# Kernel optimization log

Measured on AMD Instinct MI355X. Metric: run time of the kernel, lower is better.

Reference implementation:

```python
import jax, jax.numpy as jnp
import numpy as np

N_TOKEN = 256
C_PAIR = 128
C = 32
N_HEADS = 4
LN_EPS = 1e-5


def setup_inputs() -> dict:
    key = jax.random.key(0)
    ks = jax.random.split(key, 8)
    w = lambda k, shape: jax.random.normal(k, shape, dtype=jnp.float32) * 0.02
    return {
        "pair": jax.random.normal(ks[0], (N_TOKEN, N_TOKEN, C_PAIR), dtype=jnp.float32),
        "gamma": jnp.ones((C_PAIR,), dtype=jnp.float32),
        "beta": jnp.zeros((C_PAIR,), dtype=jnp.float32),
        "Wq": w(ks[1], (C_PAIR, C * N_HEADS)),
        "Wk": w(ks[2], (C_PAIR, C * N_HEADS)),
        "Wv": w(ks[3], (C_PAIR, C * N_HEADS)),
        "Wb": w(ks[4], (C_PAIR, N_HEADS)),
        "Wg": w(ks[5], (C_PAIR, C * N_HEADS)),
        "Wout": w(ks[6], (C * N_HEADS, C_PAIR)),
    }


def _layernorm(x, gamma, beta):
    mu = jnp.mean(x, axis=-1, keepdims=True)
    var = jnp.mean(jnp.square(x - mu), axis=-1, keepdims=True)
    return (x - mu) * jax.lax.rsqrt(var + LN_EPS) * gamma + beta


def reference(pair, gamma, beta, Wq, Wk, Wv, Wb, Wg, Wout):
    n = pair.shape[0]
    pn = _layernorm(pair, gamma, beta)  # [N, N, c_pair]
    q = (pn @ Wq).reshape(n, n, N_HEADS, C)  # [i, j, h, c]
    k = (pn @ Wk).reshape(n, n, N_HEADS, C)  # [i, k, h, c]
    v = (pn @ Wv).reshape(n, n, N_HEADS, C)
    b = pn @ Wb                               # [j, k, h] pairwise bias
    g = jax.nn.sigmoid(pn @ Wg).reshape(n, n, N_HEADS, C)
    # a^h_ijk = softmax_k( q_ij . k_ik / sqrt(c) + b_jk )
    logits = jnp.einsum("ijhc,ikhc->ijkh", q, k) / np.float32(np.sqrt(C))
    logits = logits + b[None, :, :, :]        # broadcast over i: bias indexed by (j, k)
    attn = jax.nn.softmax(logits, axis=2)     # softmax over k axis
    o = jnp.einsum("ijkh,ikhc->ijhc", attn, v) * g
    return o.reshape(n, n, N_HEADS * C) @ Wout  # [N, N, c_pair]
```

## Files before the change

### kernel.cpp

```cpp
#include <hip/hip_runtime.h>

#define N_TOK 256
#define CP    128
#define CHD   32
#define NH    4
#define NT    65536
#define NCOL  528

typedef short short8 __attribute__((ext_vector_type(8)));
typedef float f32x4  __attribute__((ext_vector_type(4)));

__device__ __forceinline__ short f2bf(float f) {
    unsigned u = __builtin_bit_cast(unsigned, f);
    u += 0x7fffu + ((u >> 16) & 1u);
    return (short)(u >> 16);
}
__device__ __forceinline__ float bf2f(short s) {
    unsigned u = ((unsigned)(unsigned short)s) << 16;
    return __builtin_bit_cast(float, u);
}

__global__ void pack_weights(const float* __restrict__ Wq, const float* __restrict__ Wk,
                             const float* __restrict__ Wv, const float* __restrict__ Wb,
                             const float* __restrict__ Wg, const float* __restrict__ Wout,
                             short* __restrict__ wcat, short* __restrict__ woutT) {
    int idx = blockIdx.x * 256 + threadIdx.x;
    if (idx < NCOL * CP) {
        int n = idx >> 7, k = idx & 127;
        float v = 0.f;
        if (n < 512) {
            const float* W = (n < 128) ? Wq : (n < 256) ? Wk : (n < 384) ? Wv : Wg;
            v = W[k * 128 + (n & 127)];
        } else if (n < 516) {
            v = Wb[k * 4 + (n - 512)];
        }
        wcat[n * CP + k] = f2bf(v);
    } else {
        int j = idx - NCOL * CP;
        if (j < 128 * 128) {
            int n = j >> 7, k = j & 127;
            woutT[n * 128 + k] = f2bf(Wout[k * 128 + n]);
        }
    }
}

__global__ __launch_bounds__(256)
void ln_proj(const float* __restrict__ pair, const float* __restrict__ gamma,
             const float* __restrict__ beta, const short* __restrict__ wcat,
             short* __restrict__ qt, short* __restrict__ kt,
             short* __restrict__ vt, short* __restrict__ gt,
             float* __restrict__ bt) {
    __shared__ short pn[64 * 136];
    const int tid = threadIdx.x;
    const int wv = tid >> 6, lane = tid & 63;
    const int quad = lane >> 4, l15 = lane & 15;
    const int r0 = blockIdx.x * 64;

    float ga0 = gamma[2 * lane], ga1 = gamma[2 * lane + 1];
    float be0 = beta[2 * lane],  be1 = beta[2 * lane + 1];

    #pragma unroll 4
    for (int rr = 0; rr < 16; ++rr) {
        int row = wv * 16 + rr;
        const float* src = pair + (size_t)(r0 + row) * CP + 2 * lane;
        float x0 = src[0], x1 = src[1];
        float s = x0 + x1;
        #pragma unroll
        for (int m = 32; m; m >>= 1) s += __shfl_xor(s, m);
        float mu = s * (1.f / 128.f);
        float d0 = x0 - mu, d1 = x1 - mu;
        float vs = d0 * d0 + d1 * d1;
        #pragma unroll
        for (int m = 32; m; m >>= 1) vs += __shfl_xor(vs, m);
        float rs = rsqrtf(vs * (1.f / 128.f) + 1e-5f);
        short y0 = f2bf(d0 * rs * ga0 + be0);
        short y1 = f2bf(d1 * rs * ga1 + be1);
        unsigned pk = ((unsigned)(unsigned short)y0) | (((unsigned)(unsigned short)y1) << 16);
        *(unsigned*)&pn[row * 136 + 2 * lane] = pk;
    }
    __syncthreads();

    short8 afrag[4];
    #pragma unroll
    for (int s = 0; s < 4; ++s)
        afrag[s] = *(const short8*)&pn[(wv * 16 + l15) * 136 + s * 32 + quad * 8];

    for (int ch = 0; ch < 33; ++ch) {
        int n = ch * 16 + l15;
        f32x4 acc = {0.f, 0.f, 0.f, 0.f};
        #pragma unroll
        for (int s = 0; s < 4; ++s) {
            short8 bfrag = *(const short8*)&wcat[(size_t)n * CP + s * 32 + quad * 8];
            acc = __builtin_amdgcn_mfma_f32_16x16x32_bf16(afrag[s], bfrag, acc, 0, 0, 0);
        }
        if (ch < 32) {
            int arr = n >> 7;
            int h = (n >> 5) & 3, c = n & 31;
            short* dst = (arr == 0) ? qt : (arr == 1) ? kt : (arr == 2) ? vt : gt;
            size_t base = (size_t)h * NT * CHD + c;
            #pragma unroll
            for (int r = 0; r < 4; ++r) {
                int gr = r0 + wv * 16 + quad * 4 + r;
                float val = acc[r];
                if (arr == 3) val = 1.f / (1.f + __expf(-val));
                dst[base + (size_t)gr * CHD] = f2bf(val);
            }
        } else if (l15 < 4) {
            int h = l15;
            #pragma unroll
            for (int r = 0; r < 4; ++r) {
                int gr = r0 + wv * 16 + quad * 4 + r;
                bt[h * NT + gr] = acc[r];
            }
        }
    }
}

__global__ __launch_bounds__(256)
void attn(const short* __restrict__ qt, const short* __restrict__ kt,
          const short* __restrict__ vt, const short* __restrict__ gt,
          const float* __restrict__ bt, short* __restrict__ og) {
    __shared__ short vT[32 * 264];
    __shared__ short pl[64 * 264];
    const int tid = threadIdx.x;
    const int h = blockIdx.x >> 8, i = blockIdx.x & 255;
    const int wv = tid >> 6, lane = tid & 63;
    const int quad = lane >> 4, l15 = lane & 15;

    const short* kbase = kt + ((size_t)h * NT + (size_t)i * 256) * CHD;
    const short* vbase = vt + ((size_t)h * NT + (size_t)i * 256) * CHD;
    const short* qbase = qt + ((size_t)h * NT + (size_t)i * 256) * CHD;
    const short* gbase = gt + ((size_t)h * NT + (size_t)i * 256) * CHD;
    const float* bbase = bt + (size_t)h * NT;

    for (int g = tid; g < 1024; g += 256) {
        int key = g >> 2, p = g & 3;
        short8 s = *(const short8*)(vbase + key * CHD + p * 8);
        #pragma unroll
        for (int cc = 0; cc < 8; ++cc)
            vT[(p * 8 + cc) * 264 + key] = s[cc];
    }
    __syncthreads();

    const float scale = 0.17677669529663687f;

    for (int jt = 0; jt < 4; ++jt) {
        int jbase = jt * 64 + wv * 16;
        short8 aq = *(const short8*)(qbase + (jbase + l15) * CHD + quad * 8);

        f32x4 sacc[16];
        #pragma unroll
        for (int t = 0; t < 16; ++t) {
            short8 bk = *(const short8*)(kbase + (t * 16 + l15) * CHD + quad * 8);
            f32x4 z = {0.f, 0.f, 0.f, 0.f};
            sacc[t] = __builtin_amdgcn_mfma_f32_16x16x32_bf16(aq, bk, z, 0, 0, 0);
        }
        #pragma unroll
        for (int t = 0; t < 16; ++t)
            #pragma unroll
            for (int r = 0; r < 4; ++r) {
                int j = jbase + quad * 4 + r;
                sacc[t][r] = sacc[t][r] * scale + bbase[(size_t)j * 256 + t * 16 + l15];
            }
        float mx[4] = {-1e30f, -1e30f, -1e30f, -1e30f}, sm[4] = {0.f, 0.f, 0.f, 0.f};
        #pragma unroll
        for (int t = 0; t < 16; ++t)
            #pragma unroll
            for (int r = 0; r < 4; ++r) mx[r] = fmaxf(mx[r], sacc[t][r]);
        #pragma unroll
        for (int m = 1; m < 16; m <<= 1)
            #pragma unroll
            for (int r = 0; r < 4; ++r) mx[r] = fmaxf(mx[r], __shfl_xor(mx[r], m, 16));
        #pragma unroll
        for (int t = 0; t < 16; ++t)
            #pragma unroll
            for (int r = 0; r < 4; ++r) {
                float e = __expf(sacc[t][r] - mx[r]);
                sacc[t][r] = e;
                sm[r] += e;
            }
        #pragma unroll
        for (int m = 1; m < 16; m <<= 1)
            #pragma unroll
            for (int r = 0; r < 4; ++r) sm[r] += __shfl_xor(sm[r], m, 16);
        float inv[4];
        #pragma unroll
        for (int r = 0; r < 4; ++r) inv[r] = 1.f / sm[r];
        #pragma unroll
        for (int t = 0; t < 16; ++t)
            #pragma unroll
            for (int r = 0; r < 4; ++r)
                pl[(wv * 16 + quad * 4 + r) * 264 + t * 16 + l15] = f2bf(sacc[t][r] * inv[r]);
        __syncthreads();
        f32x4 oacc[2];
        oacc[0] = f32x4{0.f, 0.f, 0.f, 0.f};
        oacc[1] = f32x4{0.f, 0.f, 0.f, 0.f};
        #pragma unroll
        for (int ks = 0; ks < 8; ++ks) {
            short8 ap = *(const short8*)&pl[(wv * 16 + l15) * 264 + ks * 32 + quad * 8];
            #pragma unroll
            for (int nt = 0; nt < 2; ++nt) {
                short8 bv = *(const short8*)&vT[(nt * 16 + l15) * 264 + ks * 32 + quad * 8];
                oacc[nt] = __builtin_amdgcn_mfma_f32_16x16x32_bf16(ap, bv, oacc[nt], 0, 0, 0);
            }
        }
        #pragma unroll
        for (int nt = 0; nt < 2; ++nt) {
            int c = nt * 16 + l15;
            #pragma unroll
            for (int r = 0; r < 4; ++r) {
                int j = jbase + quad * 4 + r;
                float gv = bf2f(gbase[(size_t)j * CHD + c]);
                float o = oacc[nt][r] * gv;
                og[((size_t)i * 256 + j) * CP + h * CHD + c] = f2bf(o);
            }
        }
        __syncthreads();
    }
}

__global__ __launch_bounds__(256)
void out_gemm(const short* __restrict__ og, const short* __restrict__ woutT,
              float* __restrict__ out) {
    __shared__ short al[64 * 136];
    const int tid = threadIdx.x;
    const int wv = tid >> 6, lane = tid & 63;
    const int quad = lane >> 4, l15 = lane & 15;
    const int r0 = blockIdx.x * 64;

    for (int g = tid; g < 1024; g += 256) {
        int row = g >> 4, p = g & 15;
        *(short8*)&al[row * 136 + p * 8] = *(const short8*)(og + (size_t)(r0 + row) * CP + p * 8);
    }
    __syncthreads();

    short8 af[4];
    #pragma unroll
    for (int s = 0; s < 4; ++s)
        af[s] = *(const short8*)&al[(wv * 16 + l15) * 136 + s * 32 + quad * 8];

    #pragma unroll
    for (int ch = 0; ch < 8; ++ch) {
        int n = ch * 16 + l15;
        f32x4 acc = {0.f, 0.f, 0.f, 0.f};
        #pragma unroll
        for (int s = 0; s < 4; ++s) {
            short8 bfrag = *(const short8*)&woutT[(size_t)n * 128 + s * 32 + quad * 8];
            acc = __builtin_amdgcn_mfma_f32_16x16x32_bf16(af[s], bfrag, acc, 0, 0, 0);
        }
        #pragma unroll
        for (int r = 0; r < 4; ++r)
            out[(size_t)(r0 + wv * 16 + quad * 4 + r) * CP + n] = acc[r];
    }
}

extern "C" void kernel_launch(void* const* d_in, const int* in_sizes, int n_in,
                              void* d_out, int out_size, void* d_ws, size_t ws_size,
                              hipStream_t stream) {
    (void)in_sizes; (void)n_in; (void)out_size; (void)ws_size;
    const float* pair  = (const float*)d_in[0];
    const float* gamma = (const float*)d_in[1];
    const float* beta  = (const float*)d_in[2];
    const float* Wq    = (const float*)d_in[3];
    const float* Wk    = (const float*)d_in[4];
    const float* Wv    = (const float*)d_in[5];
    const float* Wb    = (const float*)d_in[6];
    const float* Wg    = (const float*)d_in[7];
    const float* Wout  = (const float*)d_in[8];
    float* out = (float*)d_out;

    char* ws = (char*)d_ws;
    const size_t SZ_QKVG = (size_t)NH * NT * CHD * 2;
    short* wcat  = (short*)(ws);
    short* woutT = (short*)(ws + 135168);
    short* qt    = (short*)(ws + 167936);
    short* kt    = (short*)(ws + 167936 + SZ_QKVG);
    short* vt    = (short*)(ws + 167936 + 2 * SZ_QKVG);
    short* gt    = (short*)(ws + 167936 + 3 * SZ_QKVG);
    float* bt    = (float*)(ws + 167936 + 4 * SZ_QKVG);
    short* og    = (short*)(ws + 167936 + 4 * SZ_QKVG + (size_t)NH * NT * 4);

    hipLaunchKernelGGL(pack_weights, dim3(328), dim3(256), 0, stream,
                       Wq, Wk, Wv, Wb, Wg, Wout, wcat, woutT);
    hipLaunchKernelGGL(ln_proj, dim3(1024), dim3(256), 0, stream,
                       pair, gamma, beta, wcat, qt, kt, vt, gt, bt);
    hipLaunchKernelGGL(attn, dim3(1024), dim3(256), 0, stream,
                       qt, kt, vt, gt, bt, og);
    hipLaunchKernelGGL(out_gemm, dim3(1024), dim3(256), 0, stream,
                       og, woutT, out);
}
```

Baseline: 227.0 us.

## Split projection columns across waves and double-buffer weight fragments in ln_proj

Result: faster. 211.1 us (-7.0%).

```diff
diff --git a/kernel.cpp b/kernel.cpp
--- a/kernel.cpp
+++ b/kernel.cpp
@@ -44,7 +44,7 @@
     }
 }
 
-__global__ __launch_bounds__(256)
+__global__ __launch_bounds__(256, 4)
 void ln_proj(const float* __restrict__ pair, const float* __restrict__ gamma,
              const float* __restrict__ beta, const short* __restrict__ wcat,
              short* __restrict__ qt, short* __restrict__ kt,
@@ -80,40 +80,72 @@
     }
     __syncthreads();
 
-    short8 afrag[4];
+    short8 af[4][4];
     #pragma unroll
-    for (int s = 0; s < 4; ++s)
-        afrag[s] = *(const short8*)&pn[(wv * 16 + l15) * 136 + s * 32 + quad * 8];
-
-    for (int ch = 0; ch < 33; ++ch) {
-        int n = ch * 16 + l15;
-        f32x4 acc = {0.f, 0.f, 0.f, 0.f};
-        #pragma unroll
-        for (int s = 0; s < 4; ++s) {
-            short8 bfrag = *(const short8*)&wcat[(size_t)n * CP + s * 32 + quad * 8];
-            acc = __builtin_amdgcn_mfma_f32_16x16x32_bf16(afrag[s], bfrag, acc, 0, 0, 0);
-        }
-        if (ch < 32) {
-            int arr = n >> 7;
-            int h = (n >> 5) & 3, c = n & 31;
-            short* dst = (arr == 0) ? qt : (arr == 1) ? kt : (arr == 2) ? vt : gt;
-            size_t base = (size_t)h * NT * CHD + c;
-            #pragma unroll
-            for (int r = 0; r < 4; ++r) {
-                int gr = r0 + wv * 16 + quad * 4 + r;
-                float val = acc[r];
-                if (arr == 3) val = 1.f / (1.f + __expf(-val));
-                dst[base + (size_t)gr * CHD] = f2bf(val);
-            }
-        } else if (l15 < 4) {
-            int h = l15;
-            #pragma unroll
-            for (int r = 0; r < 4; ++r) {
-                int gr = r0 + wv * 16 + quad * 4 + r;
-                bt[h * NT + gr] = acc[r];
-            }
-        }
-    }
+    for (int rt = 0; rt < 4; ++rt)
+        #pragma unroll
+        for (int s = 0; s < 4; ++s)
+            af[rt][s] = *(const short8*)&pn[(rt * 16 + l15) * 136 + s * 32 + quad * 8];
+
+    short* const dst = (wv == 0) ? qt : (wv == 1) ? kt : (wv == 2) ? vt : gt;
+
+#define LOADB(BUF, CHN) {                                                          \
+        int n_ = (CHN) * 16 + l15;                                                 \
+        _Pragma("unroll")                                                          \
+        for (int s = 0; s < 4; ++s)                                                \
+            BUF[s] = *(const short8*)&wcat[(size_t)n_ * CP + s * 32 + quad * 8];   \
+    }
+
+#define CHUNK(CC, BUF) {                                                           \
+        const int chn = wv * 8 + (CC);                                             \
+        const int h_ = (chn >> 1) & 3, c_ = (chn & 1) * 16 + l15;                  \
+        const size_t base_ = (size_t)h_ * NT * CHD + c_;                           \
+        _Pragma("unroll")                                                          \
+        for (int rt = 0; rt < 4; ++rt) {                                           \
+            f32x4 acc = {0.f, 0.f, 0.f, 0.f};                                      \
+            _Pragma("unroll")                                                      \
+            for (int s = 0; s < 4; ++s)                                            \
+                acc = __builtin_amdgcn_mfma_f32_16x16x32_bf16(af[rt][s], BUF[s], acc, 0, 0, 0); \
+            _Pragma("unroll")                                                      \
+            for (int r = 0; r < 4; ++r) {                                          \
+                int gr = r0 + rt * 16 + quad * 4 + r;                              \
+                float val = acc[r];                                                \
+                if (wv == 3) val = 1.f / (1.f + __expf(-val));   \
+                dst[base_ + (size_t)gr * CHD] = f2bf(val);                         \
+            }                                                                      \
+        }                                                                          \
+    }
+
+    short8 bA[4], bB[4];
+    LOADB(bA, wv * 8 + 0)
+    LOADB(bB, wv * 8 + 1)
+    CHUNK(0, bA) LOADB(bA, wv * 8 + 2)
+    CHUNK(1, bB) LOADB(bB, wv * 8 + 3)
+    CHUNK(2, bA) LOADB(bA, wv * 8 + 4)
+    CHUNK(3, bB) LOADB(bB, wv * 8 + 5)
+    CHUNK(4, bA) LOADB(bA, wv * 8 + 6)
+    CHUNK(5, bB) LOADB(bB, wv * 8 + 7)
+    CHUNK(6, bA) LOADB(bA, wv * 8 + 8)
+    CHUNK(7, bB)
+
+    if (wv == 3) {
+        #pragma unroll
+        for (int rt = 0; rt < 4; ++rt) {
+            f32x4 acc = {0.f, 0.f, 0.f, 0.f};
+            #pragma unroll
+            for (int s = 0; s < 4; ++s)
+                acc = __builtin_amdgcn_mfma_f32_16x16x32_bf16(af[rt][s], bA[s], acc, 0, 0, 0);
+            if (l15 < 4) {
+                #pragma unroll
+                for (int r = 0; r < 4; ++r) {
+                    int gr = r0 + rt * 16 + quad * 4 + r;
+                    bt[l15 * NT + gr] = acc[r];
+                }
+            }
+        }
+    }
+#undef LOADB
+#undef CHUNK
 }
 
 __global__ __launch_bounds__(256)
```
